# Kernel optimization log

Hardware: AMD Instinct MI355X
Metric: run time of the kernel (lower is better)

The kernel has to match this reference:

```python
import jax, jax.numpy as jnp
import numpy as np

N_HEAD = 12

def setup_inputs() -> dict:
    key = jax.random.key(0)
    k1, k2, k3 = jax.random.split(key, 3)
    B, T, C = 2, 4096, 768
    x = jax.random.normal(k1, (B, T, C), dtype=jnp.float32)
    Wqkv = jax.random.normal(k2, (C, 3 * C), dtype=jnp.float32) * (1.0 / np.sqrt(C))
    bqkv = jnp.zeros((3 * C,), dtype=jnp.float32)
    Wout = jax.random.normal(k3, (C, C), dtype=jnp.float32) * (1.0 / np.sqrt(C))
    bout = jnp.zeros((C,), dtype=jnp.float32)
    return {"x": x, "Wqkv": Wqkv, "bqkv": bqkv, "Wout": Wout, "bout": bout}

def reference(x, Wqkv, bqkv, Wout, bout):
    B, T, C = x.shape
    H = N_HEAD
    D = C // H
    qkv = x @ Wqkv + bqkv                       # [B,T,3C]
    qkv = qkv.reshape(B, T, 3, H, D)
    q = qkv[:, :, 0].transpose(0, 2, 1, 3)       # [B,H,T,D]
    k = qkv[:, :, 1].transpose(0, 2, 1, 3)
    v = qkv[:, :, 2].transpose(0, 2, 1, 3)
    att = jnp.einsum('bhqd,bhkd->bhqk', q, k) / jnp.sqrt(jnp.float32(D))
    causal = jnp.tril(jnp.ones((T, T), dtype=bool))
    att = jnp.where(causal[None, None], att, jnp.float32(-jnp.inf))
    att = jax.nn.softmax(att, axis=-1)
    out = jnp.einsum('bhqk,bhkd->bhqd', att, v)  # [B,H,T,D]
    out = out.transpose(0, 2, 1, 3).reshape(B, T, C)
    return out @ Wout + bout
```

## Files before the change

### kernel.cpp

```cpp
#include <hip/hip_runtime.h>
#include <math.h>

#define Bb 2
#define Tt 4096
#define Cc 768
#define Hh 12
#define Dd 64

typedef __attribute__((ext_vector_type(8))) short short8;
typedef __attribute__((ext_vector_type(4))) float f32x4;
typedef __attribute__((ext_vector_type(4))) unsigned short u16x4;

static __device__ __forceinline__ unsigned short f2bf(float f) {
    unsigned u = __float_as_uint(f);
    u += 0x7FFF + ((u >> 16) & 1);
    return (unsigned short)(u >> 16);
}

static __device__ __forceinline__ float ex2(float x) {
    return __builtin_amdgcn_exp2f(x);
}

static __device__ __forceinline__ void gload16(const void* g, void* l) {
    __builtin_amdgcn_global_load_lds(
        (const __attribute__((address_space(1))) unsigned*)g,
        (__attribute__((address_space(3))) unsigned*)l, 16, 0, 0);
}

__global__ __launch_bounds__(256)
void prep(const float* __restrict__ x, unsigned short* __restrict__ xb,
          const float* __restrict__ Wqkv, unsigned short* __restrict__ wqkvt,
          const float* __restrict__ Wout, unsigned short* __restrict__ woutt) {
    __shared__ __align__(16) unsigned short Tl[64][72];
    const int CVT = (Bb * Tt * Cc / 8) / 256;
    const int T1  = (3 * Cc / 64) * (Cc / 64);
    int bid = blockIdx.x;

    if (bid < CVT) {
        int i = bid * 256 + threadIdx.x;
        float4 a = *(const float4*)(x + (size_t)i * 8);
        float4 b = *(const float4*)(x + (size_t)i * 8 + 4);
        union { short8 v; unsigned short u[8]; } p;
        p.u[0] = f2bf(a.x); p.u[1] = f2bf(a.y); p.u[2] = f2bf(a.z); p.u[3] = f2bf(a.w);
        p.u[4] = f2bf(b.x); p.u[5] = f2bf(b.y); p.u[6] = f2bf(b.z); p.u[7] = f2bf(b.w);
        *(short8*)(xb + (size_t)i * 8) = p.v;
        return;
    }
    bid -= CVT;
    const float* W;
    unsigned short* Wt;
    int K, N, nb, kb;
    if (bid < T1) {
        W = Wqkv; Wt = wqkvt; K = Cc; N = 3 * Cc;
        nb = bid % (3 * Cc / 64); kb = bid / (3 * Cc / 64);
    } else {
        bid -= T1;
        W = Wout; Wt = woutt; K = Cc; N = Cc;
        nb = bid % (Cc / 64); kb = bid / (Cc / 64);
    }
    int n0 = nb * 64, k0 = kb * 64;
    int t = threadIdx.x;
    int r = t >> 2, c = (t & 3) * 16;
    const float* wp = W + (size_t)(k0 + r) * N + n0 + c;
    #pragma unroll
    for (int j = 0; j < 16; j += 4) {
        float4 v = *(const float4*)(wp + j);
        Tl[c + j + 0][r] = f2bf(v.x);
        Tl[c + j + 1][r] = f2bf(v.y);
        Tl[c + j + 2][r] = f2bf(v.z);
        Tl[c + j + 3][r] = f2bf(v.w);
    }
    __syncthreads();
    unsigned short* op = Wt + (size_t)(n0 + r) * K + k0 + c;
    *(short8*)op       = *(const short8*)&Tl[r][c];
    *(short8*)(op + 8) = *(const short8*)&Tl[r][c + 8];
}

template<bool BF16OUT>
__global__ __launch_bounds__(256)
void gemm_mfma(const unsigned short* __restrict__ A, const unsigned short* __restrict__ Bt,
               const float* __restrict__ bias, void* __restrict__ Cout,
               int M, int N, int K, int qcols,
               unsigned short* __restrict__ vtb, int voff) {
    union SmemU {
        unsigned short ab[2][128][64];
        unsigned short tv[128][136];
    };
    __shared__ __align__(16) SmemU sh;
    const int tid = threadIdx.x;
    const int wid = tid >> 6, lane = tid & 63;
    const int lr = lane & 15, g = lane >> 4;
    const int wr = wid >> 1, wc = wid & 1;
    const int m0 = blockIdx.y * 128, n0 = blockIdx.x * 128;
    const int srow = lane >> 3;
    const int scol = (lane & 7) * 8;

    f32x4 acc[4][4] = {};

    for (int k0 = 0; k0 < K; k0 += 64) {
        #pragma unroll
        for (int j = 0; j < 4; ++j) {
            int ci = wid * 4 + j;
            int row = ci * 8 + srow;
            gload16(A  + (size_t)(m0 + row) * K + k0 + scol, &sh.ab[0][ci * 8][0]);
            gload16(Bt + (size_t)(n0 + row) * K + k0 + scol, &sh.ab[1][ci * 8][0]);
        }
        __syncthreads();
        #pragma unroll
        for (int ks = 0; ks < 2; ++ks) {
            short8 af[4], bfr[4];
            #pragma unroll
            for (int m = 0; m < 4; ++m)
                af[m] = *(const short8*)&sh.ab[0][wr * 64 + m * 16 + lr][ks * 32 + g * 8];
            #pragma unroll
            for (int n = 0; n < 4; ++n)
                bfr[n] = *(const short8*)&sh.ab[1][wc * 64 + n * 16 + lr][ks * 32 + g * 8];
            #pragma unroll
            for (int m = 0; m < 4; ++m)
                #pragma unroll
                for (int n = 0; n < 4; ++n)
                    acc[m][n] = __builtin_amdgcn_mfma_f32_16x16x32_bf16(
                        af[m], bfr[n], acc[m][n], 0, 0, 0);
        }
        __syncthreads();
    }

    if (vtb != nullptr && n0 >= voff) {
        #pragma unroll
        for (int n = 0; n < 4; ++n) {
            int tcol = wc * 64 + n * 16 + lr;
            float bv = bias[n0 + tcol];
            #pragma unroll
            for (int m = 0; m < 4; ++m) {
                int trow = wr * 64 + m * 16 + g * 4;
                #pragma unroll
                for (int r = 0; r < 4; ++r)
                    sh.tv[tcol][trow + r] = f2bf(acc[m][n][r] + bv);
            }
        }
        __syncthreads();
        const int dlocal = tid >> 1;
        const int th     = (tid & 1) * 64;
        const int colg   = n0 + dlocal;
        const int hd     = (colg - voff) >> 6;
        const int d      = (colg - voff) & 63;
        const int token  = m0 + th;
        const int bq     = token >> 12;
        const int t0     = token & (Tt - 1);
        unsigned short* dst = vtb + ((size_t)(bq * Hh + hd) * Dd + d) * Tt + t0;
        const unsigned short* src = &sh.tv[dlocal][th];
        #pragma unroll
        for (int j = 0; j < 8; ++j)
            *(short8*)(dst + j * 8) = *(const short8*)(src + j * 8);
        return;
    }

    const float qscale = 0.125f * 1.44269504088896340736f;
    #pragma unroll
    for (int n = 0; n < 4; ++n) {
        int coln = n0 + wc * 64 + n * 16 + lr;
        float bv = bias[coln];
        float sc = (coln < qcols) ? qscale : 1.0f;
        #pragma unroll
        for (int m = 0; m < 4; ++m) {
            int rowb = m0 + wr * 64 + m * 16 + g * 4;
            #pragma unroll
            for (int r = 0; r < 4; ++r) {
                float v = (acc[m][n][r] + bv) * sc;
                if (BF16OUT)
                    ((unsigned short*)Cout)[(size_t)(rowb + r) * N + coln] = f2bf(v);
                else
                    ((float*)Cout)[(size_t)(rowb + r) * N + coln] = v;
            }
        }
    }
}

__global__ __launch_bounds__(512)
void attn_mfma(const unsigned short* __restrict__ qkvb,
               const unsigned short* __restrict__ vtb,
               unsigned short* __restrict__ outb) {
    const int nid  = blockIdx.x;
    const int xcd  = nid & 7;
    const int rest = nid >> 3;
    const int P    = rest & 31;
    const int H2   = xcd + 8 * (rest >> 5);
    const int hd   = H2 % Hh;
    const int b    = H2 / Hh;
    const int tid = threadIdx.x;
    const int wid = tid >> 6, lane = tid & 63;
    const int strip = wid & 3, kh = wid >> 2;
    const int lr = lane & 15, g = lane >> 4;
    const int rm7 = lr & 7;
    const size_t rs = 3 * Cc;

    __shared__ __align__(16) unsigned short Ks[2][64 * 64];
    __shared__ __align__(16) unsigned short Vs[2][64 * 64];
    __shared__ __align__(16) float combO[4][64][16];
    __shared__ float combL[4][64];

    const unsigned short* qkvbase = qkvb + (size_t)b * Tt * rs;
    const unsigned short* vbase   = vtb + (size_t)((b * Hh + hd) * Dd) * Tt;

    const int row0 = tid >> 3;
    const int slog = (tid & 7) ^ (row0 & 7);
    const unsigned short* ksrc0 = qkvbase + (size_t)row0 * rs + Cc + hd * Dd + slog * 8;
    const unsigned short* vsrc0 = vbase + (size_t)row0 * Tt + slog * 8;

    const int ntA = 64 - P;
    const int qA  = (63 - P) * 64 + strip * 16 + lr;
    const int qB  = P * 64 + strip * 16 + lr;

    short8 qfA0, qfA1, qfB0, qfB1;
    {
        const unsigned short* qp = qkvbase + (size_t)qA * rs + hd * Dd;
        qfA0 = *(const short8*)(qp + g * 8);
        qfA1 = *(const short8*)(qp + 32 + g * 8);
        qp = qkvbase + (size_t)qB * rs + hd * Dd;
        qfB0 = *(const short8*)(qp + g * 8);
        qfB1 = *(const short8*)(qp + 32 + g * 8);
    }

    auto stage = [&](int buf, int ts) {
        int t = (ts < ntA) ? ts : ts - ntA;
        gload16(ksrc0 + (size_t)t * 64 * rs, &Ks[buf][wid * 512]);
        gload16(vsrc0 + t * 64,              &Vs[buf][wid * 512]);
    };

    stage(0, 0);
    __syncthreads();
    int cur = 0;

    const int laneA = lr + ((g & 1) << 5);
    const int laneB = laneA + 16;
    const int asel  = g >> 1;

    f32x4 o[4];
    #pragma unroll
    for (int dt = 0; dt < 4; ++dt) o[dt] = (f32x4){0.f, 0.f, 0.f, 0.f};
    float lpart = 0.f;
    short8 qf0 = qfA0, qf1 = qfA1;
    int myq = qA;

    auto combine_epilogue = [&]() {
        if (kh) {
            #pragma unroll
            for (int dt = 0; dt < 4; ++dt)
                *(f32x4*)&combO[strip][lane][dt * 4] = o[dt];
            combL[strip][lane] = lpart;
        }
        __syncthreads();
        if (!kh) {
            float l_r = lpart + combL[strip][lane];
            l_r += __shfl_xor(l_r, 16);
            l_r += __shfl_xor(l_r, 32);
            float inv = 1.f / fmaxf(l_r, 1e-37f);
            unsigned short* op = outb + ((size_t)b * Tt + myq) * Cc + hd * Dd + g * 4;
            #pragma unroll
            for (int dt = 0; dt < 4; ++dt) {
                f32x4 t2 = *(const f32x4*)&combO[strip][lane][dt * 4];
                u16x4 w;
                #pragma unroll
                for (int r = 0; r < 4; ++r) w[r] = f2bf((o[dt][r] + t2[r]) * inv);
                *(u16x4*)(op + dt * 16) = w;
            }
        }
        __syncthreads();
    };

    #pragma unroll 1
    for (int ts = 0; ts < 65; ++ts) {
        if (ts + 1 < 65) stage(cur ^ 1, ts + 1);

        const int inA = (ts < ntA) ? 1 : 0;
        const int kbt = inA ? ts : ts - ntA;
        const int nt  = inA ? ntA : (65 - ntA);
        const unsigned short* Kc = &Ks[cur][0];
        const unsigned short* Vc = &Vs[cur][0];

        f32x4 st[2];
        __builtin_amdgcn_s_setprio(1);
        #pragma unroll
        for (int kt = 0; kt < 2; ++kt) {
            int row = kh * 32 + kt * 16 + lr;
            int off0 = row * 64 + (g ^ rm7) * 8;
            short8 kf0 = *(const short8*)&Kc[off0];
            short8 kf1 = *(const short8*)&Kc[off0 ^ 32];
            f32x4 a = (f32x4){0.f, 0.f, 0.f, 0.f};
            a = __builtin_amdgcn_mfma_f32_16x16x32_bf16(kf0, qf0, a, 0, 0, 0);
            a = __builtin_amdgcn_mfma_f32_16x16x32_bf16(kf1, qf1, a, 0, 0, 0);
            st[kt] = a;
        }
        __builtin_amdgcn_s_setprio(0);

        if (kbt == nt - 1) {
            #pragma unroll
            for (int kt = 0; kt < 2; ++kt)
                #pragma unroll
                for (int r = 0; r < 4; ++r)
                    if (kbt * 64 + kh * 32 + kt * 16 + g * 4 + r > myq)
                        st[kt][r] = -1e30f;
        }

        float psum = 0.f;
        #pragma unroll
        for (int kt = 0; kt < 2; ++kt)
            #pragma unroll
            for (int r = 0; r < 4; ++r) {
                float p = ex2(st[kt][r]);
                st[kt][r] = p;
                psum += p;
            }
        lpart += psum;

        unsigned up[2][2];
        #pragma unroll
        for (int kt = 0; kt < 2; ++kt) {
            asm("v_cvt_pk_bf16_f32 %0, %1, %2"
                : "=v"(up[kt][0]) : "v"(st[kt][0]), "v"(st[kt][1]));
            asm("v_cvt_pk_bf16_f32 %0, %1, %2"
                : "=v"(up[kt][1]) : "v"(st[kt][2]), "v"(st[kt][3]));
        }
        {
            unsigned wa0 = __shfl(up[0][0], laneA);
            unsigned wb0 = __shfl(up[1][0], laneA);
            unsigned wa1 = __shfl(up[0][1], laneA);
            unsigned wb1 = __shfl(up[1][1], laneA);
            unsigned wa2 = __shfl(up[0][0], laneB);
            unsigned wb2 = __shfl(up[1][0], laneB);
            unsigned wa3 = __shfl(up[0][1], laneB);
            unsigned wb3 = __shfl(up[1][1], laneB);
            union { unsigned w[4]; short8 v; } pb;
            pb.w[0] = asel ? wb0 : wa0;
            pb.w[1] = asel ? wb1 : wa1;
            pb.w[2] = asel ? wb2 : wa2;
            pb.w[3] = asel ? wb3 : wa3;
            __builtin_amdgcn_s_setprio(1);
            #pragma unroll
            for (int dt = 0; dt < 4; ++dt) {
                int row = dt * 16 + lr;
                int off = row * 64 + (((kh << 2) | g) ^ rm7) * 8;
                short8 vf = *(const short8*)&Vc[off];
                o[dt] = __builtin_amdgcn_mfma_f32_16x16x32_bf16(vf, pb.v, o[dt], 0, 0, 0);
            }
            __builtin_amdgcn_s_setprio(0);
        }

        __syncthreads();
        cur ^= 1;

        if (ts == ntA - 1) {
            combine_epilogue();
            #pragma unroll
            for (int dt = 0; dt < 4; ++dt) o[dt] = (f32x4){0.f, 0.f, 0.f, 0.f};
            lpart = 0.f;
            qf0 = qfB0; qf1 = qfB1;
            myq = qB;
        }
    }

    combine_epilogue();
}

extern "C" void kernel_launch(void* const* d_in, const int* in_sizes, int n_in,
                              void* d_out, int out_size, void* d_ws, size_t ws_size,
                              hipStream_t stream) {
    const float* x    = (const float*)d_in[0];
    const float* Wqkv = (const float*)d_in[1];
    const float* bqkv = (const float*)d_in[2];
    const float* Wout = (const float*)d_in[3];
    const float* bout = (const float*)d_in[4];
    float* out = (float*)d_out;

    const int M = Bb * Tt;
    const int N1 = 3 * Cc;

    char* p = (char*)d_ws;
    unsigned short* qkvb  = (unsigned short*)p; p += (size_t)M * N1 * 2;
    unsigned short* xb    = (unsigned short*)p; p += (size_t)M * Cc * 2;
    unsigned short* wqkvt = (unsigned short*)p; p += (size_t)N1 * Cc * 2;
    unsigned short* woutt = (unsigned short*)p; p += (size_t)Cc * Cc * 2;
    unsigned short* vtb   = (unsigned short*)p; p += (size_t)Bb * Hh * Dd * Tt * 2;
    unsigned short* attb  = (unsigned short*)p; p += (size_t)M * Cc * 2;

    const int prepBlocks = (M * Cc / 8) / 256 + (N1 / 64) * (Cc / 64)
                           + (Cc / 64) * (Cc / 64);
    prep<<<dim3(prepBlocks), dim3(256), 0, stream>>>(x, xb, Wqkv, wqkvt, Wout, woutt);

    gemm_mfma<true><<<dim3(N1 / 128, M / 128), dim3(256), 0, stream>>>(
        xb, wqkvt, bqkv, qkvb, M, N1, Cc, Cc, vtb, 2 * Cc);

    attn_mfma<<<dim3(32 * Hh * Bb), dim3(512), 0, stream>>>(qkvb, vtb, attb);

    gemm_mfma<false><<<dim3(Cc / 128, M / 128), dim3(256), 0, stream>>>(
        attb, woutt, bout, out, M, Cc, Cc, 0, nullptr, 1 << 30);
}
```

Before: 191.2 us.

## Add 64x128-tile output GEMM and hoist V fragment loads in attention

Replaces the output projection with a dedicated GEMM kernel that uses 64x128 tiles, doubling the block count (6x128 instead of 6x64) so more CUs are busy for the small N=768 projection. It drops the bf16/scale/vt template paths from that launch. In the attention kernel, the V-fragment LDS reads are moved ahead of the softmax so their latency overlaps the exp and shuffle work, at the cost of extra live registers. The new GEMM is single-buffered with no LDS swizzle, so bank conflicts or exposed load latency are possible.

```diff
diff --git a/kernel.cpp b/kernel.cpp
--- a/kernel.cpp
+++ b/kernel.cpp
@@ -176,6 +176,69 @@
     }
 }
 
+__global__ __launch_bounds__(256)
+void gemm_out(const unsigned short* __restrict__ A, const unsigned short* __restrict__ Bt,
+              const float* __restrict__ bias, float* __restrict__ Cout,
+              int M, int N, int K) {
+    __shared__ __align__(16) unsigned short As[64][64];
+    __shared__ __align__(16) unsigned short Bs[128][64];
+    const int tid = threadIdx.x;
+    const int wid = tid >> 6, lane = tid & 63;
+    const int lr = lane & 15, g = lane >> 4;
+    const int wr = wid >> 1, wc = wid & 1;
+    const int m0 = blockIdx.y * 64, n0 = blockIdx.x * 128;
+    const int srow = lane >> 3;
+    const int scol = (lane & 7) * 8;
+
+    f32x4 acc[2][4] = {};
+
+    for (int k0 = 0; k0 < K; k0 += 64) {
+        #pragma unroll
+        for (int j = 0; j < 2; ++j) {
+            int ci = wid * 2 + j;
+            int row = ci * 8 + srow;
+            gload16(A + (size_t)(m0 + row) * K + k0 + scol, &As[ci * 8][0]);
+        }
+        #pragma unroll
+        for (int j = 0; j < 4; ++j) {
+            int ci = wid * 4 + j;
+            int row = ci * 8 + srow;
+            gload16(Bt + (size_t)(n0 + row) * K + k0 + scol, &Bs[ci * 8][0]);
+        }
+        __syncthreads();
+        #pragma unroll
+        for (int ks = 0; ks < 2; ++ks) {
+            short8 af[2], bfr[4];
+            #pragma unroll
+            for (int m = 0; m < 2; ++m)
+                af[m] = *(const short8*)&As[wr * 32 + m * 16 + lr][ks * 32 + g * 8];
+            #pragma unroll
+            for (int n = 0; n < 4; ++n)
+                bfr[n] = *(const short8*)&Bs[wc * 64 + n * 16 + lr][ks * 32 + g * 8];
+            #pragma unroll
+            for (int m = 0; m < 2; ++m)
+                #pragma unroll
+                for (int n = 0; n < 4; ++n)
+                    acc[m][n] = __builtin_amdgcn_mfma_f32_16x16x32_bf16(
+                        af[m], bfr[n], acc[m][n], 0, 0, 0);
+        }
+        __syncthreads();
+    }
+
+    #pragma unroll
+    for (int n = 0; n < 4; ++n) {
+        int coln = n0 + wc * 64 + n * 16 + lr;
+        float bv = bias[coln];
+        #pragma unroll
+        for (int m = 0; m < 2; ++m) {
+            int rowb = m0 + wr * 32 + m * 16 + g * 4;
+            #pragma unroll
+            for (int r = 0; r < 4; ++r)
+                Cout[(size_t)(rowb + r) * N + coln] = acc[m][n][r] + bv;
+        }
+    }
+}
+
 __global__ __launch_bounds__(512)
 void attn_mfma(const unsigned short* __restrict__ qkvb,
                const unsigned short* __restrict__ vtb,
@@ -293,6 +356,13 @@
         }
         __builtin_amdgcn_s_setprio(0);
 
+        short8 vfr[4];
+        #pragma unroll
+        for (int dt = 0; dt < 4; ++dt) {
+            int off = (dt * 16 + lr) * 64 + (((kh << 2) | g) ^ rm7) * 8;
+            vfr[dt] = *(const short8*)&Vc[off];
+        }
+
         if (kbt == nt - 1) {
             #pragma unroll
             for (int kt = 0; kt < 2; ++kt)
@@ -337,12 +407,9 @@
             pb.w[3] = asel ? wb3 : wa3;
             __builtin_amdgcn_s_setprio(1);
             #pragma unroll
-            for (int dt = 0; dt < 4; ++dt) {
-                int row = dt * 16 + lr;
-                int off = row * 64 + (((kh << 2) | g) ^ rm7) * 8;
-                short8 vf = *(const short8*)&Vc[off];
-                o[dt] = __builtin_amdgcn_mfma_f32_16x16x32_bf16(vf, pb.v, o[dt], 0, 0, 0);
-            }
+            for (int dt = 0; dt < 4; ++dt)
+                o[dt] = __builtin_amdgcn_mfma_f32_16x16x32_bf16(
+                    vfr[dt], pb.v, o[dt], 0, 0, 0);
             __builtin_amdgcn_s_setprio(0);
         }
 
@@ -392,6 +459,6 @@
 
     attn_mfma<<<dim3(32 * Hh * Bb), dim3(512), 0, stream>>>(qkvb, vtb, attb);
 
-    gemm_mfma<false><<<dim3(Cc / 128, M / 128), dim3(256), 0, stream>>>(
-        attb, woutt, bout, out, M, Cc, Cc, 0, nullptr, 1 << 30);
-}
+    gemm_out<<<dim3(Cc / 128, M / 64), dim3(256), 0, stream>>>(
+        attb, woutt, bout, out, M, Cc, Cc);
+}
```

New measurement: 222.2 us. 16.2% more time.
